# Kernel tuning notes

Measured on AMD Instinct MI355X. Metric: run time of the kernel, lower is better.

Reference implementation:

```python
import jax, jax.numpy as jnp
import numpy as np

D_MODEL = 1024
NUM_HEADS = 16
HEAD_DIM = D_MODEL // NUM_HEADS
D_FF = 4096
LN_EPS = 1e-6  # flax nnx.LayerNorm default


def setup_inputs() -> dict:
    key = jax.random.key(0)
    ks = jax.random.split(key, 13)
    s_in = 1.0 / np.sqrt(D_MODEL)
    s_ff = 1.0 / np.sqrt(D_FF)
    return {
        "x": jax.random.normal(ks[0], (2, 2048, D_MODEL), dtype=jnp.float32),
        "Wq": jax.random.normal(ks[1], (D_MODEL, D_MODEL), jnp.float32) * s_in,
        "bq": jnp.zeros((D_MODEL,), jnp.float32),
        "Wk": jax.random.normal(ks[2], (D_MODEL, D_MODEL), jnp.float32) * s_in,
        "bk": jnp.zeros((D_MODEL,), jnp.float32),
        "Wv": jax.random.normal(ks[3], (D_MODEL, D_MODEL), jnp.float32) * s_in,
        "bv": jnp.zeros((D_MODEL,), jnp.float32),
        "Wo": jax.random.normal(ks[4], (D_MODEL, D_MODEL), jnp.float32) * s_in,
        "bo": jnp.zeros((D_MODEL,), jnp.float32),
        "W1": jax.random.normal(ks[5], (D_MODEL, D_FF), jnp.float32) * s_in,
        "b1": jnp.zeros((D_FF,), jnp.float32),
        "W2": jax.random.normal(ks[6], (D_FF, D_MODEL), jnp.float32) * s_ff,
        "b2": jnp.zeros((D_MODEL,), jnp.float32),
        "ln1_scale": jnp.ones((D_MODEL,), jnp.float32),
        "ln1_bias": jnp.zeros((D_MODEL,), jnp.float32),
        "ln2_scale": jnp.ones((D_MODEL,), jnp.float32),
        "ln2_bias": jnp.zeros((D_MODEL,), jnp.float32),
    }


def layer_norm(x, scale, bias):
    mu = jnp.mean(x, axis=-1, keepdims=True)
    var = jnp.mean(jnp.square(x - mu), axis=-1, keepdims=True)
    return (x - mu) * jax.lax.rsqrt(var + LN_EPS) * scale + bias


def reference(x, Wq, bq, Wk, bk, Wv, bv, Wo, bo, W1, b1, W2, b2,
              ln1_scale, ln1_bias, ln2_scale, ln2_bias):
    B, S, _ = x.shape
    h = layer_norm(x, ln1_scale, ln1_bias)
    # project and split heads: [B, H, S, Dh]
    q = (h @ Wq + bq).reshape(B, S, NUM_HEADS, HEAD_DIM).transpose(0, 2, 1, 3)
    k = (h @ Wk + bk).reshape(B, S, NUM_HEADS, HEAD_DIM).transpose(0, 2, 1, 3)
    v = (h @ Wv + bv).reshape(B, S, NUM_HEADS, HEAD_DIM).transpose(0, 2, 1, 3)
    scores = jnp.einsum("bhqd,bhkd->bhqk", q, k) / jnp.sqrt(jnp.float32(HEAD_DIM))
    attn = jax.nn.softmax(scores, axis=-1)
    out = jnp.einsum("bhqk,bhkd->bhqd", attn, v)
    out = out.transpose(0, 2, 1, 3).reshape(B, S, D_MODEL)
    x = x + out @ Wo + bo
    h2 = layer_norm(x, ln2_scale, ln2_bias)
    ff = jax.nn.relu(h2 @ W1 + b1) @ W2 + b2
    return x + ff
```

## Files before the change

### kernel.cpp

```cpp
#include <hip/hip_runtime.h>

typedef unsigned short ushort_t;
typedef __attribute__((ext_vector_type(8))) __bf16 bf16x8;
typedef __attribute__((ext_vector_type(8))) unsigned short ushort8v;
typedef __attribute__((ext_vector_type(4))) float floatx4;

__device__ inline float b2f(ushort_t u) {
    union { unsigned int i; float f; } c; c.i = ((unsigned int)u) << 16; return c.f;
}
__device__ inline ushort_t f2b(float f) {
    union { float f; unsigned int i; } c; c.f = f;
    unsigned int i = c.i;
    unsigned int r = (i + 0x7FFFu + ((i >> 16) & 1u)) >> 16;
    return (ushort_t)r;
}
__device__ inline bf16x8 as_bf16x8(ushort8v u) { return __builtin_bit_cast(bf16x8, u); }

__global__ __launch_bounds__(256) void concat3_kernel(
    const float* __restrict__ a, const float* __restrict__ b,
    const float* __restrict__ c, float* __restrict__ o) {
    int t = blockIdx.x * 256 + threadIdx.x;
    if (t < 3072)
        o[t] = t < 1024 ? a[t] : (t < 2048 ? b[t - 1024] : c[t - 2048]);
}

__global__ __launch_bounds__(256) void copy_f32_kernel(
    const float* __restrict__ src, float* __restrict__ dst) {
    size_t i = ((size_t)blockIdx.x * 256 + threadIdx.x) * 4;
    *(float4*)(dst + i) = *(const float4*)(src + i);
}

__global__ __launch_bounds__(256) void transpose_conv_kernel(
    const float* __restrict__ in, ushort_t* __restrict__ out,
    int R, int Csub, int ldin) {
    __shared__ float tile[32][33];
    int tx = threadIdx.x, ty = threadIdx.y;
    int r0 = blockIdx.y * 32, c0 = blockIdx.x * 32;
#pragma unroll
    for (int i = 0; i < 32; i += 8)
        tile[ty + i][tx] = in[(size_t)(r0 + ty + i) * ldin + c0 + tx];
    __syncthreads();
#pragma unroll
    for (int i = 0; i < 32; i += 8)
        out[(size_t)(c0 + ty + i) * R + r0 + tx] = f2b(tile[tx][ty + i]);
}

__global__ __launch_bounds__(256) void transpose_v_kernel(
    const ushort_t* __restrict__ qkv, ushort_t* __restrict__ vt) {
    __shared__ ushort_t tile[32][33];
    int tx = threadIdx.x, ty = threadIdx.y;
    int s0 = blockIdx.x * 32, d0 = blockIdx.y * 32;
    int bh = blockIdx.z, b = bh >> 4, h = bh & 15;
    const ushort_t* src = qkv + (size_t)b * 2048 * 3072 + 2048 + h * 64;
    ushort_t* dst = vt + (size_t)bh * 64 * 2048;
#pragma unroll
    for (int i = 0; i < 32; i += 8)
        tile[ty + i][tx] = src[(size_t)(s0 + ty + i) * 3072 + d0 + tx];
    __syncthreads();
#pragma unroll
    for (int i = 0; i < 32; i += 8)
        dst[(size_t)(d0 + ty + i) * 2048 + s0 + tx] = tile[tx][ty + i];
}

__device__ inline float wave_sum(float s) {
#pragma unroll
    for (int o = 32; o > 0; o >>= 1) s += __shfl_xor(s, o);
    return s;
}

__global__ __launch_bounds__(256) void ln_f32_kernel(
    const float* __restrict__ x, const float* __restrict__ sc,
    const float* __restrict__ bi, ushort_t* __restrict__ out) {
    int row = blockIdx.x, t = threadIdx.x;
    const float* xr = x + (size_t)row * 1024;
    float4 u = *(const float4*)(xr + t * 4);
    float v0 = u.x, v1 = u.y, v2 = u.z, v3 = u.w;
    __shared__ float sm[8];
    int wv = t >> 6, lane = t & 63;
    float s = wave_sum(v0 + v1 + v2 + v3);
    if (lane == 0) sm[wv] = s;
    __syncthreads();
    float mean = (sm[0] + sm[1] + sm[2] + sm[3]) * (1.0f / 1024.0f);
    float d0 = v0 - mean, d1 = v1 - mean, d2 = v2 - mean, d3 = v3 - mean;
    float q = wave_sum(d0 * d0 + d1 * d1 + d2 * d2 + d3 * d3);
    if (lane == 0) sm[4 + wv] = q;
    __syncthreads();
    float var = (sm[4] + sm[5] + sm[6] + sm[7]) * (1.0f / 1024.0f);
    float rn = rsqrtf(var + 1e-6f);
    float4 us = *(const float4*)(sc + t * 4);
    float4 ub = *(const float4*)(bi + t * 4);
    ushort4 o;
    o.x = f2b(d0 * rn * us.x + ub.x);
    o.y = f2b(d1 * rn * us.y + ub.y);
    o.z = f2b(d2 * rn * us.z + ub.z);
    o.w = f2b(d3 * rn * us.w + ub.w);
    *(ushort4*)(out + (size_t)row * 1024 + t * 4) = o;
}

__global__ __launch_bounds__(256) void gemm_bt_kernel(
    const ushort_t* __restrict__ A, const ushort_t* __restrict__ Bt,
    const float* __restrict__ bias, const float* __restrict__ resf,
    ushort_t* __restrict__ Cb, float* __restrict__ Cf,
    int M, int N, int K, int ldb, int op) {
    __shared__ __align__(16) ushort_t As[128 * 40];
    __shared__ __align__(16) ushort_t Bs[128 * 40];
    int tid = threadIdx.x;
    int m0 = blockIdx.y * 128, n0 = blockIdx.x * 128;
    int wv = tid >> 6, lane = tid & 63;
    int wr = wv & 1, wc = wv >> 1;
    int mo = wr * 64, no = wc * 64;
    int quad = lane >> 4, l16 = lane & 15;
    int k8 = quad * 8;

    floatx4 acc[4][4] = {};

    for (int k0 = 0; k0 < K; k0 += 32) {
#pragma unroll
        for (int c = 0; c < 2; ++c) {
            int e = c * 2048 + tid * 8;
            int r = e >> 5, kk = e & 31;
            *(ushort8v*)(As + r * 40 + kk) = *(const ushort8v*)(A + (size_t)(m0 + r) * K + k0 + kk);
            *(ushort8v*)(Bs + r * 40 + kk) = *(const ushort8v*)(Bt + (size_t)(n0 + r) * ldb + k0 + kk);
        }
        __syncthreads();
        bf16x8 af[4], bfr[4];
#pragma unroll
        for (int i = 0; i < 4; ++i) {
            af[i]  = as_bf16x8(*(const ushort8v*)(As + (mo + i * 16 + l16) * 40 + k8));
            bfr[i] = as_bf16x8(*(const ushort8v*)(Bs + (no + i * 16 + l16) * 40 + k8));
        }
#pragma unroll
        for (int mi = 0; mi < 4; ++mi)
#pragma unroll
            for (int ni = 0; ni < 4; ++ni)
                acc[mi][ni] = __builtin_amdgcn_mfma_f32_16x16x32_bf16(
                    af[mi], bfr[ni], acc[mi][ni], 0, 0, 0);
        __syncthreads();
    }

#pragma unroll
    for (int mi = 0; mi < 4; ++mi) {
#pragma unroll
        for (int r = 0; r < 4; ++r) {
            int row = m0 + mo + mi * 16 + quad * 4 + r;
            size_t rowoff = (size_t)row * N;
#pragma unroll
            for (int ni = 0; ni < 4; ++ni) {
                int col = n0 + no + ni * 16 + l16;
                float val = acc[mi][ni][r];
                if (op != 3) val += bias[col];
                if (op == 1) val = fmaxf(val, 0.0f);
                if (op >= 2) {
                    val += resf[rowoff + col];
                    Cf[rowoff + col] = val;
                } else {
                    Cb[rowoff + col] = f2b(val);
                }
            }
        }
    }
}

__global__ __launch_bounds__(256) void gemm_bt_atomic_kernel(
    const ushort_t* __restrict__ A, const ushort_t* __restrict__ Bt,
    const float* __restrict__ bias, float* __restrict__ Cf,
    int M, int N, int lda, int ldb, int Kc) {
    __shared__ __align__(16) ushort_t As[128 * 40];
    __shared__ __align__(16) ushort_t Bs[128 * 40];
    int tid = threadIdx.x;
    int m0 = blockIdx.y * 128, n0 = blockIdx.x * 128;
    int kbase = blockIdx.z * Kc;
    int wv = tid >> 6, lane = tid & 63;
    int wr = wv & 1, wc = wv >> 1;
    int mo = wr * 64, no = wc * 64;
    int quad = lane >> 4, l16 = lane & 15;
    int k8 = quad * 8;

    floatx4 acc[4][4] = {};

    for (int k0 = kbase; k0 < kbase + Kc; k0 += 32) {
#pragma unroll
        for (int c = 0; c < 2; ++c) {
            int e = c * 2048 + tid * 8;
            int r = e >> 5, kk = e & 31;
            *(ushort8v*)(As + r * 40 + kk) = *(const ushort8v*)(A + (size_t)(m0 + r) * lda + k0 + kk);
            *(ushort8v*)(Bs + r * 40 + kk) = *(const ushort8v*)(Bt + (size_t)(n0 + r) * ldb + k0 + kk);
        }
        __syncthreads();
        bf16x8 af[4], bfr[4];
#pragma unroll
        for (int i = 0; i < 4; ++i) {
            af[i]  = as_bf16x8(*(const ushort8v*)(As + (mo + i * 16 + l16) * 40 + k8));
            bfr[i] = as_bf16x8(*(const ushort8v*)(Bs + (no + i * 16 + l16) * 40 + k8));
        }
#pragma unroll
        for (int mi = 0; mi < 4; ++mi)
#pragma unroll
            for (int ni = 0; ni < 4; ++ni)
                acc[mi][ni] = __builtin_amdgcn_mfma_f32_16x16x32_bf16(
                    af[mi], bfr[ni], acc[mi][ni], 0, 0, 0);
        __syncthreads();
    }

    bool addb = (blockIdx.z == 0) && (bias != nullptr);
#pragma unroll
    for (int mi = 0; mi < 4; ++mi) {
#pragma unroll
        for (int r = 0; r < 4; ++r) {
            int row = m0 + mo + mi * 16 + quad * 4 + r;
            size_t rowoff = (size_t)row * N;
#pragma unroll
            for (int ni = 0; ni < 4; ++ni) {
                int col = n0 + no + ni * 16 + l16;
                float val = acc[mi][ni][r];
                if (addb) val += bias[col];
                unsafeAtomicAdd(&Cf[rowoff + col], val);
            }
        }
    }
}

__global__ __launch_bounds__(256) void attn_kernel(
    const ushort_t* __restrict__ qkv, const ushort_t* __restrict__ vt,
    ushort_t* __restrict__ om) {
    const int LDQ = 3072, LDO = 1024;
    int bh = blockIdx.y;
    int b = bh >> 4, h = bh & 15;
    size_t qbase = (size_t)b * 2048 * LDQ + h * 64;
    size_t kbase = qbase + 1024;
    const ushort_t* vtp = vt + (size_t)bh * 64 * 2048;
    int q0 = blockIdx.x * 128;
    int tid = threadIdx.x, wv = tid >> 6, lane = tid & 63;
    int quad = lane >> 4, l16 = lane & 15;
    int k8 = quad * 8;

    __shared__ __align__(16) ushort_t Ks[64 * 72];
    __shared__ __align__(16) ushort_t Vs[64 * 72];
    __shared__ __align__(16) ushort_t Ps[4 * 32 * 76];
    ushort_t* ps = Ps + wv * 32 * 76;

    int sr0 = tid >> 3, scc0 = (tid & 7) * 8;
    int sr1 = sr0 + 32;

    bf16x8 qf[2][2];
#pragma unroll
    for (int mt = 0; mt < 2; ++mt) {
        const ushort_t* qptr = qkv + qbase + (size_t)(q0 + wv * 32 + mt * 16 + l16) * LDQ;
        qf[mt][0] = as_bf16x8(*(const ushort8v*)(qptr + k8));
        qf[mt][1] = as_bf16x8(*(const ushort8v*)(qptr + 32 + k8));
    }

    bf16x8 ones;
#pragma unroll
    for (int j = 0; j < 8; ++j) ones[j] = (__bf16)1.0f;

    floatx4 Oacc[2][4] = {};
    floatx4 lsum[2] = {};

    ushort8v kreg0, kreg1, vreg0, vreg1;
    kreg0 = *(const ushort8v*)(qkv + kbase + (size_t)sr0 * LDQ + scc0);
    kreg1 = *(const ushort8v*)(qkv + kbase + (size_t)sr1 * LDQ + scc0);
    vreg0 = *(const ushort8v*)(vtp + (size_t)sr0 * 2048 + scc0);
    vreg1 = *(const ushort8v*)(vtp + (size_t)sr1 * 2048 + scc0);

    for (int kb = 0; kb < 2048; kb += 64) {
        __syncthreads();
        *(ushort8v*)(Ks + sr0 * 72 + scc0) = kreg0;
        *(ushort8v*)(Ks + sr1 * 72 + scc0) = kreg1;
        *(ushort8v*)(Vs + sr0 * 72 + scc0) = vreg0;
        *(ushort8v*)(Vs + sr1 * 72 + scc0) = vreg1;
        __syncthreads();

        int nkb = (kb + 64 < 2048) ? kb + 64 : 0;
        kreg0 = *(const ushort8v*)(qkv + kbase + (size_t)(nkb + sr0) * LDQ + scc0);
        kreg1 = *(const ushort8v*)(qkv + kbase + (size_t)(nkb + sr1) * LDQ + scc0);
        vreg0 = *(const ushort8v*)(vtp + (size_t)sr0 * 2048 + nkb + scc0);
        vreg1 = *(const ushort8v*)(vtp + (size_t)sr1 * 2048 + nkb + scc0);

        bf16x8 kf[4][2];
#pragma unroll
        for (int kt = 0; kt < 4; ++kt)
#pragma unroll
            for (int ds = 0; ds < 2; ++ds)
                kf[kt][ds] = as_bf16x8(
                    *(const ushort8v*)(Ks + (kt * 16 + l16) * 72 + ds * 32 + k8));

        floatx4 sc[2][4];
#pragma unroll
        for (int mt = 0; mt < 2; ++mt)
#pragma unroll
            for (int kt = 0; kt < 4; ++kt) {
                floatx4 s = {0.0f, 0.0f, 0.0f, 0.0f};
                s = __builtin_amdgcn_mfma_f32_16x16x32_bf16(qf[mt][0], kf[kt][0], s, 0, 0, 0);
                s = __builtin_amdgcn_mfma_f32_16x16x32_bf16(qf[mt][1], kf[kt][1], s, 0, 0, 0);
                sc[mt][kt] = s;
            }

#pragma unroll
        for (int mt = 0; mt < 2; ++mt)
#pragma unroll
            for (int kt = 0; kt < 4; ++kt)
#pragma unroll
                for (int r = 0; r < 4; ++r)
                    ps[(mt * 16 + quad * 4 + r) * 76 + kt * 16 + l16] =
                        f2b(__expf(sc[mt][kt][r] * 0.125f));

        bf16x8 vf[4][2];
#pragma unroll
        for (int dt = 0; dt < 4; ++dt)
#pragma unroll
            for (int ks = 0; ks < 2; ++ks)
                vf[dt][ks] = as_bf16x8(
                    *(const ushort8v*)(Vs + (dt * 16 + l16) * 72 + ks * 32 + k8));
#pragma unroll
        for (int mt = 0; mt < 2; ++mt) {
            bf16x8 pf0 = as_bf16x8(*(const ushort8v*)(ps + (mt * 16 + l16) * 76 + k8));
            bf16x8 pf1 = as_bf16x8(*(const ushort8v*)(ps + (mt * 16 + l16) * 76 + 32 + k8));
#pragma unroll
            for (int dt = 0; dt < 4; ++dt) {
                Oacc[mt][dt] = __builtin_amdgcn_mfma_f32_16x16x32_bf16(pf0, vf[dt][0], Oacc[mt][dt], 0, 0, 0);
                Oacc[mt][dt] = __builtin_amdgcn_mfma_f32_16x16x32_bf16(pf1, vf[dt][1], Oacc[mt][dt], 0, 0, 0);
            }
            lsum[mt] = __builtin_amdgcn_mfma_f32_16x16x32_bf16(pf0, ones, lsum[mt], 0, 0, 0);
            lsum[mt] = __builtin_amdgcn_mfma_f32_16x16x32_bf16(pf1, ones, lsum[mt], 0, 0, 0);
        }
    }

#pragma unroll
    for (int mt = 0; mt < 2; ++mt)
#pragma unroll
        for (int r = 0; r < 4; ++r) {
            float inv = 1.0f / lsum[mt][r];
            size_t rowoff = (size_t)(b * 2048 + q0 + wv * 32 + mt * 16 + quad * 4 + r) * LDO + h * 64;
#pragma unroll
            for (int dt = 0; dt < 4; ++dt)
                om[rowoff + dt * 16 + l16] = f2b(Oacc[mt][dt][r] * inv);
        }
}

extern "C" void kernel_launch(void* const* d_in, const int* in_sizes, int n_in,
                              void* d_out, int out_size, void* d_ws, size_t ws_size,
                              hipStream_t stream) {
    const float* x    = (const float*)d_in[0];
    const float* Wq   = (const float*)d_in[1];
    const float* bq   = (const float*)d_in[2];
    const float* Wk   = (const float*)d_in[3];
    const float* bk   = (const float*)d_in[4];
    const float* Wv   = (const float*)d_in[5];
    const float* bv   = (const float*)d_in[6];
    const float* Wo   = (const float*)d_in[7];
    const float* bo   = (const float*)d_in[8];
    const float* W1   = (const float*)d_in[9];
    const float* b1   = (const float*)d_in[10];
    const float* W2   = (const float*)d_in[11];
    const float* b2   = (const float*)d_in[12];
    const float* ln1s = (const float*)d_in[13];
    const float* ln1b = (const float*)d_in[14];
    const float* ln2s = (const float*)d_in[15];
    const float* ln2b = (const float*)d_in[16];
    float*    outf = (float*)d_out;
    ushort_t* ws   = (ushort_t*)d_ws;

    const size_t M1 = 1048576;
    ushort_t* qkvT    = ws;
    ushort_t* WoT     = ws + 3 * M1;
    ushort_t* W1T     = ws + 4 * M1;
    ushort_t* W2T     = ws + 8 * M1;
    ushort_t* h       = ws + 12 * M1;
    ushort_t* attnout = ws + 12 * M1;
    ushort_t* qkv     = ws + 16 * M1;
    ushort_t* h2      = ws;
    ushort_t* ffbuf   = ws + 12 * M1;
    float*    bqkv    = (float*)d_out;
    ushort_t* vtbuf   = (ushort_t*)d_out;

    dim3 tb(32, 8);
    dim3 tg(32, 32);

    concat3_kernel<<<12, 256, 0, stream>>>(bq, bk, bv, bqkv);
    transpose_conv_kernel<<<tg, tb, 0, stream>>>(Wq, qkvT,           1024, 1024, 1024);
    transpose_conv_kernel<<<tg, tb, 0, stream>>>(Wk, qkvT + 1 * M1,  1024, 1024, 1024);
    transpose_conv_kernel<<<tg, tb, 0, stream>>>(Wv, qkvT + 2 * M1,  1024, 1024, 1024);
    transpose_conv_kernel<<<tg, tb, 0, stream>>>(Wo, WoT,            1024, 1024, 1024);
    transpose_conv_kernel<<<dim3(128, 32), tb, 0, stream>>>(W1, W1T, 1024, 4096, 4096);
    transpose_conv_kernel<<<dim3(32, 128), tb, 0, stream>>>(W2, W2T, 4096, 1024, 1024);

    ln_f32_kernel<<<4096, 256, 0, stream>>>(x, ln1s, ln1b, h);

    gemm_bt_kernel<<<dim3(24, 32), 256, 0, stream>>>(
        h, qkvT, bqkv, nullptr, qkv, nullptr, 4096, 3072, 1024, 1024, 0);

    transpose_v_kernel<<<dim3(64, 2, 32), tb, 0, stream>>>(qkv, vtbuf);

    attn_kernel<<<dim3(16, 32), 256, 0, stream>>>(qkv, vtbuf, attnout);

    copy_f32_kernel<<<4096, 256, 0, stream>>>(x, outf);
    gemm_bt_atomic_kernel<<<dim3(8, 32, 4), 256, 0, stream>>>(
        attnout, WoT, bo, outf, 4096, 1024, 1024, 1024, 256);

    ln_f32_kernel<<<4096, 256, 0, stream>>>(outf, ln2s, ln2b, h2);

    gemm_bt_kernel<<<dim3(32, 32), 256, 0, stream>>>(
        h2, W1T, b1, nullptr, ffbuf, nullptr, 4096, 4096, 1024, 1024, 1);

    gemm_bt_atomic_kernel<<<dim3(8, 32, 4), 256, 0, stream>>>(
        ffbuf, W2T, b2, outf, 4096, 1024, 4096, 4096, 1024);
}
```

Measured before the change: 538.7 us.

## Use direct global-to-LDS loads in GEMMs and halve attention query tile

The GEMM kernels now stage A and B tiles through global_load_lds, a direct global-to-LDS path that bypasses registers, and drop the row padding (stride 40 to 32) to match its contiguous per-wave layout. This aims to cut register pressure and the VGPR round-trip of the load/store staging. The unpadded layout may bring LDS bank conflicts on the MFMA fragment reads. Separately, the attention kernel handles 64 queries per block instead of 128, doubling the grid to 1024 blocks for more parallelism and fewer registers, at the cost of reloading K/V tiles twice as often.

```diff
diff --git a/kernel.cpp b/kernel.cpp
--- a/kernel.cpp
+++ b/kernel.cpp
@@ -15,6 +15,12 @@
     return (ushort_t)r;
 }
 __device__ inline bf16x8 as_bf16x8(ushort8v u) { return __builtin_bit_cast(bf16x8, u); }
+
+__device__ inline void load_lds16(const ushort_t* g, ushort_t* l) {
+    __builtin_amdgcn_global_load_lds(
+        (const __attribute__((address_space(1))) void*)g,
+        (__attribute__((address_space(3))) void*)l, 16, 0, 0);
+}
 
 __global__ __launch_bounds__(256) void concat3_kernel(
     const float* __restrict__ a, const float* __restrict__ b,
@@ -102,8 +108,8 @@
     const float* __restrict__ bias, const float* __restrict__ resf,
     ushort_t* __restrict__ Cb, float* __restrict__ Cf,
     int M, int N, int K, int ldb, int op) {
-    __shared__ __align__(16) ushort_t As[128 * 40];
-    __shared__ __align__(16) ushort_t Bs[128 * 40];
+    __shared__ __align__(16) ushort_t As[128 * 32];
+    __shared__ __align__(16) ushort_t Bs[128 * 32];
     int tid = threadIdx.x;
     int m0 = blockIdx.y * 128, n0 = blockIdx.x * 128;
     int wv = tid >> 6, lane = tid & 63;
@@ -119,15 +125,16 @@
         for (int c = 0; c < 2; ++c) {
             int e = c * 2048 + tid * 8;
             int r = e >> 5, kk = e & 31;
-            *(ushort8v*)(As + r * 40 + kk) = *(const ushort8v*)(A + (size_t)(m0 + r) * K + k0 + kk);
-            *(ushort8v*)(Bs + r * 40 + kk) = *(const ushort8v*)(Bt + (size_t)(n0 + r) * ldb + k0 + kk);
+            int wbase = c * 2048 + wv * 512;
+            load_lds16(A + (size_t)(m0 + r) * K + k0 + kk, As + wbase);
+            load_lds16(Bt + (size_t)(n0 + r) * ldb + k0 + kk, Bs + wbase);
         }
         __syncthreads();
         bf16x8 af[4], bfr[4];
 #pragma unroll
         for (int i = 0; i < 4; ++i) {
-            af[i]  = as_bf16x8(*(const ushort8v*)(As + (mo + i * 16 + l16) * 40 + k8));
-            bfr[i] = as_bf16x8(*(const ushort8v*)(Bs + (no + i * 16 + l16) * 40 + k8));
+            af[i]  = as_bf16x8(*(const ushort8v*)(As + (mo + i * 16 + l16) * 32 + k8));
+            bfr[i] = as_bf16x8(*(const ushort8v*)(Bs + (no + i * 16 + l16) * 32 + k8));
         }
 #pragma unroll
         for (int mi = 0; mi < 4; ++mi)
@@ -165,8 +172,8 @@
     const ushort_t* __restrict__ A, const ushort_t* __restrict__ Bt,
     const float* __restrict__ bias, float* __restrict__ Cf,
     int M, int N, int lda, int ldb, int Kc) {
-    __shared__ __align__(16) ushort_t As[128 * 40];
-    __shared__ __align__(16) ushort_t Bs[128 * 40];
+    __shared__ __align__(16) ushort_t As[128 * 32];
+    __shared__ __align__(16) ushort_t Bs[128 * 32];
     int tid = threadIdx.x;
     int m0 = blockIdx.y * 128, n0 = blockIdx.x * 128;
     int kbase = blockIdx.z * Kc;
@@ -183,15 +190,16 @@
         for (int c = 0; c < 2; ++c) {
             int e = c * 2048 + tid * 8;
             int r = e >> 5, kk = e & 31;
-            *(ushort8v*)(As + r * 40 + kk) = *(const ushort8v*)(A + (size_t)(m0 + r) * lda + k0 + kk);
-            *(ushort8v*)(Bs + r * 40 + kk) = *(const ushort8v*)(Bt + (size_t)(n0 + r) * ldb + k0 + kk);
+            int wbase = c * 2048 + wv * 512;
+            load_lds16(A + (size_t)(m0 + r) * lda + k0 + kk, As + wbase);
+            load_lds16(Bt + (size_t)(n0 + r) * ldb + k0 + kk, Bs + wbase);
         }
         __syncthreads();
         bf16x8 af[4], bfr[4];
 #pragma unroll
         for (int i = 0; i < 4; ++i) {
-            af[i]  = as_bf16x8(*(const ushort8v*)(As + (mo + i * 16 + l16) * 40 + k8));
-            bfr[i] = as_bf16x8(*(const ushort8v*)(Bs + (no + i * 16 + l16) * 40 + k8));
+            af[i]  = as_bf16x8(*(const ushort8v*)(As + (mo + i * 16 + l16) * 32 + k8));
+            bfr[i] = as_bf16x8(*(const ushort8v*)(Bs + (no + i * 16 + l16) * 32 + k8));
         }
 #pragma unroll
         for (int mi = 0; mi < 4; ++mi)
@@ -229,33 +237,32 @@
     size_t qbase = (size_t)b * 2048 * LDQ + h * 64;
     size_t kbase = qbase + 1024;
     const ushort_t* vtp = vt + (size_t)bh * 64 * 2048;
-    int q0 = blockIdx.x * 128;
+    int q0 = blockIdx.x * 64;
     int tid = threadIdx.x, wv = tid >> 6, lane = tid & 63;
     int quad = lane >> 4, l16 = lane & 15;
     int k8 = quad * 8;
 
     __shared__ __align__(16) ushort_t Ks[64 * 72];
     __shared__ __align__(16) ushort_t Vs[64 * 72];
-    __shared__ __align__(16) ushort_t Ps[4 * 32 * 76];
-    ushort_t* ps = Ps + wv * 32 * 76;
+    __shared__ __align__(16) ushort_t Ps[4 * 16 * 76];
+    ushort_t* ps = Ps + wv * 16 * 76;
 
     int sr0 = tid >> 3, scc0 = (tid & 7) * 8;
     int sr1 = sr0 + 32;
 
-    bf16x8 qf[2][2];
-#pragma unroll
-    for (int mt = 0; mt < 2; ++mt) {
-        const ushort_t* qptr = qkv + qbase + (size_t)(q0 + wv * 32 + mt * 16 + l16) * LDQ;
-        qf[mt][0] = as_bf16x8(*(const ushort8v*)(qptr + k8));
-        qf[mt][1] = as_bf16x8(*(const ushort8v*)(qptr + 32 + k8));
+    bf16x8 qf[2];
+    {
+        const ushort_t* qptr = qkv + qbase + (size_t)(q0 + wv * 16 + l16) * LDQ;
+        qf[0] = as_bf16x8(*(const ushort8v*)(qptr + k8));
+        qf[1] = as_bf16x8(*(const ushort8v*)(qptr + 32 + k8));
     }
 
     bf16x8 ones;
 #pragma unroll
     for (int j = 0; j < 8; ++j) ones[j] = (__bf16)1.0f;
 
-    floatx4 Oacc[2][4] = {};
-    floatx4 lsum[2] = {};
+    floatx4 Oacc[4] = {};
+    floatx4 lsum = {};
 
     ushort8v kreg0, kreg1, vreg0, vreg1;
     kreg0 = *(const ushort8v*)(qkv + kbase + (size_t)sr0 * LDQ + scc0);
@@ -277,65 +284,45 @@
         vreg0 = *(const ushort8v*)(vtp + (size_t)sr0 * 2048 + nkb + scc0);
         vreg1 = *(const ushort8v*)(vtp + (size_t)sr1 * 2048 + nkb + scc0);
 
-        bf16x8 kf[4][2];
+        floatx4 sc[4];
+#pragma unroll
+        for (int kt = 0; kt < 4; ++kt) {
+            bf16x8 kf0 = as_bf16x8(*(const ushort8v*)(Ks + (kt * 16 + l16) * 72 + k8));
+            bf16x8 kf1 = as_bf16x8(*(const ushort8v*)(Ks + (kt * 16 + l16) * 72 + 32 + k8));
+            floatx4 s = {0.0f, 0.0f, 0.0f, 0.0f};
+            s = __builtin_amdgcn_mfma_f32_16x16x32_bf16(qf[0], kf0, s, 0, 0, 0);
+            s = __builtin_amdgcn_mfma_f32_16x16x32_bf16(qf[1], kf1, s, 0, 0, 0);
+            sc[kt] = s;
+        }
+
 #pragma unroll
         for (int kt = 0; kt < 4; ++kt)
 #pragma unroll
-            for (int ds = 0; ds < 2; ++ds)
-                kf[kt][ds] = as_bf16x8(
-                    *(const ushort8v*)(Ks + (kt * 16 + l16) * 72 + ds * 32 + k8));
-
-        floatx4 sc[2][4];
-#pragma unroll
-        for (int mt = 0; mt < 2; ++mt)
-#pragma unroll
-            for (int kt = 0; kt < 4; ++kt) {
-                floatx4 s = {0.0f, 0.0f, 0.0f, 0.0f};
-                s = __builtin_amdgcn_mfma_f32_16x16x32_bf16(qf[mt][0], kf[kt][0], s, 0, 0, 0);
-                s = __builtin_amdgcn_mfma_f32_16x16x32_bf16(qf[mt][1], kf[kt][1], s, 0, 0, 0);
-                sc[mt][kt] = s;
-            }
-
-#pragma unroll
-        for (int mt = 0; mt < 2; ++mt)
-#pragma unroll
-            for (int kt = 0; kt < 4; ++kt)
-#pragma unroll
-                for (int r = 0; r < 4; ++r)
-                    ps[(mt * 16 + quad * 4 + r) * 76 + kt * 16 + l16] =
-                        f2b(__expf(sc[mt][kt][r] * 0.125f));
-
-        bf16x8 vf[4][2];
+            for (int r = 0; r < 4; ++r)
+                ps[(quad * 4 + r) * 76 + kt * 16 + l16] =
+                    f2b(__expf(sc[kt][r] * 0.125f));
+
+        bf16x8 pf0 = as_bf16x8(*(const ushort8v*)(ps + l16 * 76 + k8));
+        bf16x8 pf1 = as_bf16x8(*(const ushort8v*)(ps + l16 * 76 + 32 + k8));
+#pragma unroll
+        for (int dt = 0; dt < 4; ++dt) {
+            bf16x8 vf0 = as_bf16x8(*(const ushort8v*)(Vs + (dt * 16 + l16) * 72 + k8));
+            bf16x8 vf1 = as_bf16x8(*(const ushort8v*)(Vs + (dt * 16 + l16) * 72 + 32 + k8));
+            Oacc[dt] = __builtin_amdgcn_mfma_f32_16x16x32_bf16(pf0, vf0, Oacc[dt], 0, 0, 0);
+            Oacc[dt] = __builtin_amdgcn_mfma_f32_16x16x32_bf16(pf1, vf1, Oacc[dt], 0, 0, 0);
+        }
+        lsum = __builtin_amdgcn_mfma_f32_16x16x32_bf16(pf0, ones, lsum, 0, 0, 0);
+        lsum = __builtin_amdgcn_mfma_f32_16x16x32_bf16(pf1, ones, lsum, 0, 0, 0);
+    }
+
+#pragma unroll
+    for (int r = 0; r < 4; ++r) {
+        float inv = 1.0f / lsum[r];
+        size_t rowoff = (size_t)(b * 2048 + q0 + wv * 16 + quad * 4 + r) * LDO + h * 64;
 #pragma unroll
         for (int dt = 0; dt < 4; ++dt)
-#pragma unroll
-            for (int ks = 0; ks < 2; ++ks)
-                vf[dt][ks] = as_bf16x8(
-                    *(const ushort8v*)(Vs + (dt * 16 + l16) * 72 + ks * 32 + k8));
-#pragma unroll
-        for (int mt = 0; mt < 2; ++mt) {
-            bf16x8 pf0 = as_bf16x8(*(const ushort8v*)(ps + (mt * 16 + l16) * 76 + k8));
-            bf16x8 pf1 = as_bf16x8(*(const ushort8v*)(ps + (mt * 16 + l16) * 76 + 32 + k8));
-#pragma unroll
-            for (int dt = 0; dt < 4; ++dt) {
-                Oacc[mt][dt] = __builtin_amdgcn_mfma_f32_16x16x32_bf16(pf0, vf[dt][0], Oacc[mt][dt], 0, 0, 0);
-                Oacc[mt][dt] = __builtin_amdgcn_mfma_f32_16x16x32_bf16(pf1, vf[dt][1], Oacc[mt][dt], 0, 0, 0);
-            }
-            lsum[mt] = __builtin_amdgcn_mfma_f32_16x16x32_bf16(pf0, ones, lsum[mt], 0, 0, 0);
-            lsum[mt] = __builtin_amdgcn_mfma_f32_16x16x32_bf16(pf1, ones, lsum[mt], 0, 0, 0);
-        }
-    }
-
-#pragma unroll
-    for (int mt = 0; mt < 2; ++mt)
-#pragma unroll
-        for (int r = 0; r < 4; ++r) {
-            float inv = 1.0f / lsum[mt][r];
-            size_t rowoff = (size_t)(b * 2048 + q0 + wv * 32 + mt * 16 + quad * 4 + r) * LDO + h * 64;
-#pragma unroll
-            for (int dt = 0; dt < 4; ++dt)
-                om[rowoff + dt * 16 + l16] = f2b(Oacc[mt][dt][r] * inv);
-        }
+            om[rowoff + dt * 16 + l16] = f2b(Oacc[dt][r] * inv);
+    }
 }
 
 extern "C" void kernel_launch(void* const* d_in, const int* in_sizes, int n_in,
@@ -392,7 +379,7 @@
 
     transpose_v_kernel<<<dim3(64, 2, 32), tb, 0, stream>>>(qkv, vtbuf);
 
-    attn_kernel<<<dim3(16, 32), 256, 0, stream>>>(qkv, vtbuf, attnout);
+    attn_kernel<<<dim3(32, 32), 256, 0, stream>>>(qkv, vtbuf, attnout);
 
     copy_f32_kernel<<<4096, 256, 0, stream>>>(x, outf);
     gemm_bt_atomic_kernel<<<dim3(8, 32, 4), 256, 0, stream>>>(
```

Measured after the change: 533.8 us. About the same (-0.9%).
